# Kernel optimization log

Measured on AMD Instinct MI355X. Metric: run time of the kernel, lower is better.

## Reference

```python
import jax, jax.numpy as jnp
import numpy as np

T_CONST = 0.1

def _hardtanh(w):
    # F.hardtanh(w, min_val=1e-10, max_val=1)
    return jnp.clip(w, 1e-10, 1.0)

def _forward(inp, hn, w_str2str, w_str2snr, w_m12m1, w_m12str, w_thal2m1,
             w_m12thal, w_thal2str, w_str2stn, w_stn2snr, w_snr2thal,
             str2str_fixed, inp_weight, mean_w, mean_b, std_w, std_b, hid_dim):
    H = hid_dim
    H5 = 5 * H
    Z = jnp.zeros((H, H), dtype=inp.dtype)
    n_inhib = int(0.3 * H)

    # Diagonal 'D' matrices realized as column scalings (D is diagonal)
    m12m1_d = jnp.concatenate([jnp.ones((H - n_inhib,)), -jnp.ones((n_inhib,))])

    # Block masks
    str2str_mask = jnp.zeros((H, H))
    m12str_mask = jnp.concatenate([jnp.ones((H, H - n_inhib)), jnp.zeros((H, n_inhib))], axis=1)
    str2stn_mask = jnp.concatenate([jnp.zeros((H, H // 2)), jnp.ones((H, H // 2))], axis=1)
    str2snr_mask = jnp.concatenate([jnp.ones((H, H // 2)), jnp.zeros((H, H // 2))], axis=1)

    # Region masks over the full 5H state
    thal_mask = jnp.concatenate([jnp.zeros((3 * H,)), jnp.ones((H,)), jnp.zeros((H,))])
    m1_mask = jnp.zeros((H5,))  # cat(zeros(4H), zeros(H)) in the source

    # Effective recurrent blocks (str2str_D = stn2snr_D = snr2thal_D = str2snr_D = -I)
    str2str_rec = -(str2str_mask * _hardtanh(w_str2str) + str2str_fixed)
    m12m1_rec = _hardtanh(w_m12m1) * m12m1_d[None, :]
    m12str_rec = m12str_mask * _hardtanh(w_m12str)
    str2snr_rec = -(str2snr_mask * _hardtanh(w_str2snr))
    thal2m1_rec = _hardtanh(w_thal2m1)
    m12thal_rec = _hardtanh(w_m12thal)
    thal2str_rec = _hardtanh(w_thal2str)
    str2stn_rec = str2stn_mask * _hardtanh(w_str2stn)
    stn2snr_rec = -_hardtanh(w_str2stn)  # NOTE: source uses str2stn weight here (faithful to original)
    snr2thal_rec = -_hardtanh(w_snr2thal)

    W_rec = jnp.concatenate([
        jnp.concatenate([str2str_rec, Z, Z, thal2str_rec, m12str_rec], axis=1),
        jnp.concatenate([str2stn_rec, Z, Z, Z, Z], axis=1),
        jnp.concatenate([str2snr_rec, stn2snr_rec, Z, Z, Z], axis=1),
        jnp.concatenate([Z, Z, snr2thal_rec, Z, m12thal_rec], axis=1),
        jnp.concatenate([Z, Z, Z, thal2m1_rec, m12m1_rec], axis=1),
    ], axis=0)  # [5H, 5H]

    # Precompute masked input drive for all timesteps: [T, B, 5H]
    u = jnp.einsum('bti,ih->tbh', inp, _hardtanh(inp_weight)) * thal_mask

    W_rec_T = W_rec.T

    def step(h, u_t):
        # (W_rec @ h.T).T == h @ W_rec.T
        h_new = jax.nn.relu((1.0 - T_CONST) * h + T_CONST * (h @ W_rec_T + u_t))
        return h_new, h_new

    _, hs = jax.lax.scan(step, hn[0], u)  # hs: [T, B, 5H]
    rnn_out = jnp.transpose(hs, (1, 0, 2))  # [B, T, 5H]
    hn_last = rnn_out[:, -1, :][None]  # [1, B, 5H]

    masked = rnn_out * m1_mask
    mean_out = masked @ mean_w + mean_b
    std_out = jnp.clip(masked @ std_w + std_b, -5.0, 10.0)
    return mean_out, std_out, rnn_out, hn_last


def setup_inputs() -> dict:
    H, B, T, I, A = 256, 64, 512, 4, 1
    H5 = 5 * H
    key = jax.random.key(0)
    ks = jax.random.split(key, 20)
    u01 = lambda k, shape, s: jax.random.uniform(k, shape, dtype=jnp.float32) * s
    inputs = {
        'inp': jax.random.uniform(ks[0], (B, T, I), dtype=jnp.float32),
        'hn': jnp.zeros((1, B, H5), dtype=jnp.float32),
        'w_str2str': u01(ks[1], (H, H), 0.01),
        'w_str2snr': u01(ks[2], (H, H), 0.01),
        'w_m12m1': u01(ks[3], (H, H), 0.01),
        'w_m12str': u01(ks[4], (H, H), 0.01),
        'w_thal2m1': u01(ks[5], (H, H), 0.01),
        'w_m12thal': u01(ks[6], (H, H), 0.01),
        'w_thal2str': u01(ks[7], (H, H), 0.01),
        'w_str2stn': u01(ks[8], (H, H), 0.01),
        'w_stn2snr': u01(ks[9], (H, H), 0.01),
        'w_snr2thal': u01(ks[10], (H, H), 0.01),
        'inp_weight': u01(ks[12], (I, H5), 0.1),
        'mean_w': jax.random.normal(ks[13], (H5, A), dtype=jnp.float32) * 0.02,
        'mean_b': jnp.zeros((A,), dtype=jnp.float32),
        'std_w': jax.random.normal(ks[14], (H5, A), dtype=jnp.float32) * 0.02,
        'std_b': jnp.zeros((A,), dtype=jnp.float32),
        'hid_dim': H,
    }
    keep = jax.random.bernoulli(ks[11], 0.15, (H, H)).astype(jnp.float32)
    inputs['str2str_fixed'] = u01(ks[15], (H, H), 0.01) * keep
    return inputs


def reference(inp, hn, w_str2str, w_str2snr, w_m12m1, w_m12str, w_thal2m1,
              w_m12thal, w_thal2str, w_str2stn, w_stn2snr, w_snr2thal,
              str2str_fixed, inp_weight, mean_w, mean_b, std_w, std_b, hid_dim):
    return _forward(inp, hn, w_str2str, w_str2snr, w_m12m1, w_m12str, w_thal2m1,
                    w_m12thal, w_thal2str, w_str2stn, w_stn2snr, w_snr2thal,
                    str2str_fixed, inp_weight, mean_w, mean_b, std_w, std_b, hid_dim)
```

## Files before the change

### kernel.cpp

```cpp
#include <hip/hip_runtime.h>

typedef unsigned short u16;
typedef unsigned long long u64;
typedef __bf16 v8bf __attribute__((ext_vector_type(8)));
typedef float f32x4 __attribute__((ext_vector_type(4)));
typedef u16 u16x4 __attribute__((ext_vector_type(4)));

#define H5 1280
#define TT 512
#define NBLK 80
#define SPL 81920

#define OFF_W0 0
#define OFF_W1 3276800
#define OFF_W2 6553600
#define OFF_HS 9830400
#define OFF_WIN 10813440
#define OFF_CNT 10817536

#define MFMA(a, b, c) __builtin_amdgcn_mfma_f32_16x16x32_bf16(a, b, c, 0, 0, 0)

__device__ __forceinline__ float htanh_(float x) {
  return fminf(fmaxf(x, 1e-10f), 1.0f);
}
__device__ __forceinline__ u16 f2b(float f) {
  unsigned u = __float_as_uint(f);
  return (u16)((u + 0x7fffu + ((u >> 16) & 1u)) >> 16);
}
__device__ __forceinline__ float b2f(u16 b) {
  return __uint_as_float(((unsigned)b) << 16);
}

__device__ __forceinline__ v8bf ldh(const u16* p) {
  union { u64 q[2]; v8bf v; } u;
  u.q[0] = __hip_atomic_load((const u64*)p, __ATOMIC_RELAXED, __HIP_MEMORY_SCOPE_AGENT);
  u.q[1] = __hip_atomic_load((const u64*)(p + 4), __ATOMIC_RELAXED, __HIP_MEMORY_SCOPE_AGENT);
  return u.v;
}
__device__ __forceinline__ void sth(u16* p, u16x4 v) {
  union { u16x4 s; u64 q; } u;
  u.s = v;
  __hip_atomic_store((u64*)p, u.q, __ATOMIC_RELAXED, __HIP_MEMORY_SCOPE_AGENT);
}

__global__ void build_w(const float* __restrict__ w_str2snr, const float* __restrict__ w_m12m1,
                        const float* __restrict__ w_m12str, const float* __restrict__ w_thal2m1,
                        const float* __restrict__ w_m12thal, const float* __restrict__ w_thal2str,
                        const float* __restrict__ w_str2stn, const float* __restrict__ w_snr2thal,
                        const float* __restrict__ fixedw, u16* __restrict__ W0,
                        u16* __restrict__ W1, u16* __restrict__ W2) {
  int idx = blockIdx.x * 256 + threadIdx.x;
  if (idx >= H5 * H5) return;
  int j = idx / H5, k = idx - j * H5;
  int jr = j >> 8, kr = k >> 8, kk = k & 255;
  int o = (j & 255) * 256 + kk;
  float w = 0.0f;
  if (jr == 0) {
    if (kr == 0) w = -fixedw[o];
    else if (kr == 3) w = htanh_(w_thal2str[o]);
    else if (kr == 4) w = (kk < 180) ? htanh_(w_m12str[o]) : 0.0f;
  } else if (jr == 1) {
    if (kr == 0) w = (kk >= 128) ? htanh_(w_str2stn[o]) : 0.0f;
  } else if (jr == 2) {
    if (kr == 0) w = (kk < 128) ? -htanh_(w_str2snr[o]) : 0.0f;
    else if (kr == 1) w = -htanh_(w_str2stn[o]);
  } else if (jr == 3) {
    if (kr == 2) w = -htanh_(w_snr2thal[o]);
    else if (kr == 4) w = htanh_(w_m12thal[o]);
  } else {
    if (kr == 3) w = htanh_(w_thal2m1[o]);
    else if (kr == 4) w = (kk < 180) ? htanh_(w_m12m1[o]) : -htanh_(w_m12m1[o]);
  }
  u16 c0 = f2b(w);  float r1 = w - b2f(c0);
  u16 c1 = f2b(r1); float r2 = r1 - b2f(c1);
  u16 c2 = f2b(r2);
  W0[idx] = c0; W1[idx] = c1; W2[idx] = c2;
}

__global__ void build_misc(const float* __restrict__ hn, const float* __restrict__ inp_weight,
                           const float* __restrict__ mean_b, const float* __restrict__ std_b,
                           float* __restrict__ out, u16* __restrict__ hs, float* __restrict__ Win) {
  int gid = blockIdx.x * 256 + threadIdx.x;
  if (gid < 65536) {
    out[gid] = (gid < 32768) ? mean_b[0] : fminf(10.0f, fmaxf(-5.0f, std_b[0]));
  } else if (gid < 65536 + SPL) {
    int i = gid - 65536;
    float v = hn[i];
    u16 c0 = f2b(v);  float r1 = v - b2f(c0);
    u16 c1 = f2b(r1); float r2 = r1 - b2f(c1);
    u16 c2 = f2b(r2);
    hs[i] = c0; hs[SPL + i] = c1; hs[2 * SPL + i] = c2;
  } else if (gid < 65536 + SPL + 1024) {
    int i = gid - 65536 - SPL;
    Win[i] = htanh_(inp_weight[(i >> 8) * H5 + 768 + (i & 255)]);
  }
}

template <int R> struct RC;
template <> struct RC<0> { static constexpr int kb[3] = {0, 768, 1024}; static constexpr int nch[3] = {8, 8, 8}; };
template <> struct RC<1> { static constexpr int kb[3] = {128, 0, 0};    static constexpr int nch[3] = {4, 0, 0}; };
template <> struct RC<2> { static constexpr int kb[3] = {0, 256, 0};    static constexpr int nch[3] = {4, 8, 0}; };
template <> struct RC<3> { static constexpr int kb[3] = {512, 1024, 0}; static constexpr int nch[3] = {8, 8, 0}; };
template <> struct RC<4> { static constexpr int kb[3] = {768, 1024, 0}; static constexpr int nch[3] = {8, 8, 0}; };
template <int R> constexpr int NCT = RC<R>::nch[0] + RC<R>::nch[1] + RC<R>::nch[2];

template <int R>
__device__ __forceinline__ void load_afr_t(const u16* __restrict__ W0, const u16* __restrict__ W1,
                                           const u16* __restrict__ W2, int j0, int lr, int lk,
                                           v8bf (&afr)[NCT<R>][3]) {
  const long jrow = (long)(j0 + lr) * H5 + lk;
  int idx = 0;
#pragma unroll
  for (int q = 0; q < 3; ++q) {
#pragma unroll
    for (int c = 0; c < RC<R>::nch[q]; ++c) {
      long off = jrow + RC<R>::kb[q] + c * 32;
      afr[idx][0] = *(const v8bf*)(W0 + off);
      afr[idx][1] = *(const v8bf*)(W1 + off);
      afr[idx][2] = *(const v8bf*)(W2 + off);
      ++idx;
    }
  }
}

template <int R>
__device__ __forceinline__ f32x4 mfma_step_t(const u16* __restrict__ hs_r, int b, int lk,
                                             const v8bf (&afr)[NCT<R>][3]) {
  f32x4 a00 = {0.f, 0.f, 0.f, 0.f}, a01 = {0.f, 0.f, 0.f, 0.f};
  f32x4 a10 = {0.f, 0.f, 0.f, 0.f}, a11 = {0.f, 0.f, 0.f, 0.f};
  int idx = 0;
#pragma unroll
  for (int q = 0; q < 3; ++q) {
    if (RC<R>::nch[q] > 0) {
      const u16* hb = hs_r + (long)b * H5 + RC<R>::kb[q] + lk;
#pragma unroll
      for (int c = 0; c < RC<R>::nch[q]; ++c) {
        v8bf h0 = ldh(hb + c * 32);
        v8bf h1 = ldh(hb + SPL + c * 32);
        v8bf h2 = ldh(hb + 2 * SPL + c * 32);
        if (idx & 1) {
          a10 = MFMA(afr[idx][0], h0, a10);
          a11 = MFMA(afr[idx][0], h1, a11);
          a10 = MFMA(afr[idx][1], h0, a10);
          a11 = MFMA(afr[idx][1], h1, a11);
          a10 = MFMA(afr[idx][2], h0, a10);
          a11 = MFMA(afr[idx][0], h2, a11);
        } else {
          a00 = MFMA(afr[idx][0], h0, a00);
          a01 = MFMA(afr[idx][0], h1, a01);
          a00 = MFMA(afr[idx][1], h0, a00);
          a01 = MFMA(afr[idx][1], h1, a01);
          a00 = MFMA(afr[idx][2], h0, a00);
          a01 = MFMA(afr[idx][0], h2, a01);
        }
        ++idx;
      }
    }
  }
  f32x4 acc;
#pragma unroll
  for (int rr = 0; rr < 4; ++rr) acc[rr] = (a00[rr] + a01[rr]) + (a10[rr] + a11[rr]);
  return acc;
}

template <int R>
__device__ void pers_loop(int j0, int b, int lr, int hi, int lk,
                          const float* __restrict__ inp_b, const float* __restrict__ hn,
                          const u16* __restrict__ W0, const u16* __restrict__ W1,
                          const u16* __restrict__ W2, u16* __restrict__ hs,
                          float* __restrict__ rnn_b, float* __restrict__ hn_last,
                          const float* __restrict__ Win, unsigned* __restrict__ counter) {
  v8bf afr[NCT<R>][3];
  load_afr_t<R>(W0, W1, W2, j0, lr, lk, afr);

  float winreg[4][4];
  if constexpr (R == 3) {
#pragma unroll
    for (int i = 0; i < 4; ++i)
#pragma unroll
      for (int rr = 0; rr < 4; ++rr)
        winreg[i][rr] = Win[i * 256 + (j0 - 768) + hi * 4 + rr];
  }

  f32x4 hprev;
  {
    const float* hp = hn + (long)b * H5 + j0 + hi * 4;
#pragma unroll
    for (int rr = 0; rr < 4; ++rr) hprev[rr] = hp[rr];
  }

  const u64 ca = (u64)counter;

  for (int t = 0; t < TT; ++t) {
    const u16* hs_r = hs + (t & 1) * (3 * SPL);
    u16* hs_w = hs + ((t & 1) ^ 1) * (3 * SPL);

    f32x4 acc = mfma_step_t<R>(hs_r, b, lk, afr);

    if constexpr (R == 3) {
      const float* ip = inp_b + t * 4;
      float i0 = ip[0], i1 = ip[1], i2 = ip[2], i3 = ip[3];
#pragma unroll
      for (int rr = 0; rr < 4; ++rr)
        acc[rr] += i0 * winreg[0][rr] + i1 * winreg[1][rr] + i2 * winreg[2][rr] + i3 * winreg[3][rr];
    }

    f32x4 hnew;
#pragma unroll
    for (int rr = 0; rr < 4; ++rr)
      hnew[rr] = fmaxf(0.0f, 0.9f * hprev[rr] + 0.1f * acc[rr]);
    hprev = hnew;

    *(f32x4*)(rnn_b + (long)t * H5 + j0 + hi * 4) = hnew;

    if (t < TT - 1) {
      u16x4 s0, s1, s2;
#pragma unroll
      for (int rr = 0; rr < 4; ++rr) {
        float v = hnew[rr];
        u16 c0 = f2b(v);  float r1 = v - b2f(c0);
        u16 c1 = f2b(r1); float r2 = r1 - b2f(c1);
        s0[rr] = c0; s1[rr] = c1; s2[rr] = f2b(r2);
      }
      u16* hw = hs_w + (long)b * H5 + j0 + hi * 4;
      sth(hw, s0);
      sth(hw + SPL, s1);
      sth(hw + 2 * SPL, s2);

      asm volatile("s_waitcnt vmcnt(0)" ::: "memory");
      __syncthreads();
      if (threadIdx.x == 0) {
        unsigned old;
        asm volatile("global_atomic_add %0, %1, %2, off sc0 sc1\n\t"
                     "s_waitcnt vmcnt(0)"
                     : "=v"(old) : "v"(ca), "v"(1u) : "memory");
        const unsigned target = (unsigned)(t + 1) * NBLK;
        for (;;) {
          unsigned cur;
          asm volatile("global_load_dword %0, %1, off sc0 sc1\n\t"
                       "s_waitcnt vmcnt(0)"
                       : "=v"(cur) : "v"(ca) : "memory");
          if (cur >= target) break;
          __builtin_amdgcn_s_sleep(1);
        }
      }
      __syncthreads();
    } else {
      float* hl = hn_last + (long)b * H5 + j0 + hi * 4;
#pragma unroll
      for (int rr = 0; rr < 4; ++rr) hl[rr] = hnew[rr];
    }
  }
}

__global__ void __launch_bounds__(256, 1)
rnn_pers(const float* __restrict__ inp, const float* __restrict__ hn,
         const u16* __restrict__ W0, const u16* __restrict__ W1, const u16* __restrict__ W2,
         u16* __restrict__ hs, float* __restrict__ rnn, float* __restrict__ hn_last,
         const float* __restrict__ Win, unsigned* __restrict__ counter) {
  const int lane = threadIdx.x & 63;
  const int lr = lane & 15, hi = lane >> 4, lk = hi * 8;
  const int jt = blockIdx.x;
  const int bt = threadIdx.x >> 6;
  const int j0 = jt << 4;
  const int b = (bt << 4) + lr;
  float* rnn_b = rnn + (long)b * TT * H5;
  const float* inp_b = inp + (long)b * TT * 4;
  switch (jt >> 4) {
    case 0: pers_loop<0>(j0, b, lr, hi, lk, inp_b, hn, W0, W1, W2, hs, rnn_b, hn_last, Win, counter); break;
    case 1: pers_loop<1>(j0, b, lr, hi, lk, inp_b, hn, W0, W1, W2, hs, rnn_b, hn_last, Win, counter); break;
    case 2: pers_loop<2>(j0, b, lr, hi, lk, inp_b, hn, W0, W1, W2, hs, rnn_b, hn_last, Win, counter); break;
    case 3: pers_loop<3>(j0, b, lr, hi, lk, inp_b, hn, W0, W1, W2, hs, rnn_b, hn_last, Win, counter); break;
    default: pers_loop<4>(j0, b, lr, hi, lk, inp_b, hn, W0, W1, W2, hs, rnn_b, hn_last, Win, counter); break;
  }
}

template <int R>
__device__ void step_one(int t, int j0, int b, int lr, int hi, int lk,
                         const float* __restrict__ inp_b, const float* __restrict__ hn,
                         const u16* __restrict__ W0, const u16* __restrict__ W1,
                         const u16* __restrict__ W2, u16* __restrict__ hs,
                         float* __restrict__ rnn, float* __restrict__ rnn_b,
                         float* __restrict__ hn_last, const float* __restrict__ Win) {
  v8bf afr[NCT<R>][3];
  load_afr_t<R>(W0, W1, W2, j0, lr, lk, afr);
  float winreg[4][4];
  if constexpr (R == 3) {
#pragma unroll
    for (int i = 0; i < 4; ++i)
#pragma unroll
      for (int rr = 0; rr < 4; ++rr)
        winreg[i][rr] = Win[i * 256 + (j0 - 768) + hi * 4 + rr];
  }
  f32x4 hprev;
  {
    const float* hp = (t == 0) ? (hn + (long)b * H5 + j0 + hi * 4)
                               : (rnn + ((long)b * TT + (t - 1)) * H5 + j0 + hi * 4);
#pragma unroll
    for (int rr = 0; rr < 4; ++rr) hprev[rr] = hp[rr];
  }
  const u16* hs_r = hs + (t & 1) * (3 * SPL);
  u16* hs_w = hs + ((t & 1) ^ 1) * (3 * SPL);

  f32x4 acc = mfma_step_t<R>(hs_r, b, lk, afr);
  if constexpr (R == 3) {
    const float* ip = inp_b + t * 4;
    float i0 = ip[0], i1 = ip[1], i2 = ip[2], i3 = ip[3];
#pragma unroll
    for (int rr = 0; rr < 4; ++rr)
      acc[rr] += i0 * winreg[0][rr] + i1 * winreg[1][rr] + i2 * winreg[2][rr] + i3 * winreg[3][rr];
  }
  f32x4 hnew;
#pragma unroll
  for (int rr = 0; rr < 4; ++rr)
    hnew[rr] = fmaxf(0.0f, 0.9f * hprev[rr] + 0.1f * acc[rr]);

  *(f32x4*)(rnn_b + (long)t * H5 + j0 + hi * 4) = hnew;
  if (t < TT - 1) {
    u16x4 s0, s1, s2;
#pragma unroll
    for (int rr = 0; rr < 4; ++rr) {
      float v = hnew[rr];
      u16 c0 = f2b(v);  float r1 = v - b2f(c0);
      u16 c1 = f2b(r1); float r2 = r1 - b2f(c1);
      s0[rr] = c0; s1[rr] = c1; s2[rr] = f2b(r2);
    }
    u16* hw = hs_w + (long)b * H5 + j0 + hi * 4;
    sth(hw, s0);
    sth(hw + SPL, s1);
    sth(hw + 2 * SPL, s2);
  } else {
    float* hl = hn_last + (long)b * H5 + j0 + hi * 4;
#pragma unroll
    for (int rr = 0; rr < 4; ++rr) hl[rr] = hnew[rr];
  }
}

__global__ void __launch_bounds__(256, 1)
rnn_step(const float* __restrict__ inp, const float* __restrict__ hn,
         const u16* __restrict__ W0, const u16* __restrict__ W1, const u16* __restrict__ W2,
         u16* __restrict__ hs, float* __restrict__ rnn, float* __restrict__ hn_last,
         const float* __restrict__ Win, int t) {
  const int lane = threadIdx.x & 63;
  const int lr = lane & 15, hi = lane >> 4, lk = hi * 8;
  const int jt = blockIdx.x;
  const int bt = threadIdx.x >> 6;
  const int j0 = jt << 4;
  const int b = (bt << 4) + lr;
  float* rnn_b = rnn + (long)b * TT * H5;
  const float* inp_b = inp + (long)b * TT * 4;
  switch (jt >> 4) {
    case 0: step_one<0>(t, j0, b, lr, hi, lk, inp_b, hn, W0, W1, W2, hs, rnn, rnn_b, hn_last, Win); break;
    case 1: step_one<1>(t, j0, b, lr, hi, lk, inp_b, hn, W0, W1, W2, hs, rnn, rnn_b, hn_last, Win); break;
    case 2: step_one<2>(t, j0, b, lr, hi, lk, inp_b, hn, W0, W1, W2, hs, rnn, rnn_b, hn_last, Win); break;
    case 3: step_one<3>(t, j0, b, lr, hi, lk, inp_b, hn, W0, W1, W2, hs, rnn, rnn_b, hn_last, Win); break;
    default: step_one<4>(t, j0, b, lr, hi, lk, inp_b, hn, W0, W1, W2, hs, rnn, rnn_b, hn_last, Win); break;
  }
}

extern "C" void kernel_launch(void* const* d_in, const int* in_sizes, int n_in,
                              void* d_out, int out_size, void* d_ws, size_t ws_size,
                              hipStream_t stream) {
  const float* inp        = (const float*)d_in[0];
  const float* hn         = (const float*)d_in[1];
  const float* w_str2snr  = (const float*)d_in[3];
  const float* w_m12m1    = (const float*)d_in[4];
  const float* w_m12str   = (const float*)d_in[5];
  const float* w_thal2m1  = (const float*)d_in[6];
  const float* w_m12thal  = (const float*)d_in[7];
  const float* w_thal2str = (const float*)d_in[8];
  const float* w_str2stn  = (const float*)d_in[9];
  const float* w_snr2thal = (const float*)d_in[11];
  const float* inp_weight = (const float*)d_in[12];
  const float* mean_b     = (const float*)d_in[14];
  const float* std_b      = (const float*)d_in[16];
  const float* fixedw     = (const float*)d_in[18];

  char* ws = (char*)d_ws;
  u16* W0 = (u16*)(ws + OFF_W0);
  u16* W1 = (u16*)(ws + OFF_W1);
  u16* W2 = (u16*)(ws + OFF_W2);
  u16* hsb = (u16*)(ws + OFF_HS);
  float* Win = (float*)(ws + OFF_WIN);
  unsigned* cnt = (unsigned*)(ws + OFF_CNT);

  float* out = (float*)d_out;
  float* rnn = out + 65536;
  float* hnl = out + 65536 + 41943040;

  hipMemsetAsync(cnt, 0, 128, stream);
  build_w<<<6400, 256, 0, stream>>>(w_str2snr, w_m12m1, w_m12str, w_thal2m1, w_m12thal,
                                    w_thal2str, w_str2stn, w_snr2thal, fixedw, W0, W1, W2);
  build_misc<<<581, 256, 0, stream>>>(hn, inp_weight, mean_b, std_b, out, hsb, Win);

  void* args[] = {(void*)&inp, (void*)&hn, (void*)&W0, (void*)&W1, (void*)&W2, (void*)&hsb,
                  (void*)&rnn, (void*)&hnl, (void*)&Win, (void*)&cnt};
  hipError_t e = hipLaunchCooperativeKernel((const void*)rnn_pers, dim3(NBLK), dim3(256),
                                            args, 0, stream);
  if (e != hipSuccess) {
    for (int t = 0; t < TT; ++t)
      rnn_step<<<NBLK, 256, 0, stream>>>(inp, hn, W0, W1, W2, hsb, rnn, hnl, Win, t);
  }
}
```

Before: 10.02 ms.

## Stream weight fragments from memory each step instead of holding them in registers

Measured after the change: 10.20 ms. No clear change (+1.8%).

```diff
diff --git a/kernel.cpp b/kernel.cpp
--- a/kernel.cpp
+++ b/kernel.cpp
@@ -31,7 +31,7 @@
   return __uint_as_float(((unsigned)b) << 16);
 }
 
-__device__ __forceinline__ v8bf ldh(const u16* p) {
+__device__ __forceinline__ v8bf ald16(const u16* p) {
   union { u64 q[2]; v8bf v; } u;
   u.q[0] = __hip_atomic_load((const u64*)p, __ATOMIC_RELAXED, __HIP_MEMORY_SCOPE_AGENT);
   u.q[1] = __hip_atomic_load((const u64*)(p + 4), __ATOMIC_RELAXED, __HIP_MEMORY_SCOPE_AGENT);
@@ -102,64 +102,39 @@
 template <> struct RC<2> { static constexpr int kb[3] = {0, 256, 0};    static constexpr int nch[3] = {4, 8, 0}; };
 template <> struct RC<3> { static constexpr int kb[3] = {512, 1024, 0}; static constexpr int nch[3] = {8, 8, 0}; };
 template <> struct RC<4> { static constexpr int kb[3] = {768, 1024, 0}; static constexpr int nch[3] = {8, 8, 0}; };
-template <int R> constexpr int NCT = RC<R>::nch[0] + RC<R>::nch[1] + RC<R>::nch[2];
 
 template <int R>
-__device__ __forceinline__ void load_afr_t(const u16* __restrict__ W0, const u16* __restrict__ W1,
-                                           const u16* __restrict__ W2, int j0, int lr, int lk,
-                                           v8bf (&afr)[NCT<R>][3]) {
-  const long jrow = (long)(j0 + lr) * H5 + lk;
-  int idx = 0;
-#pragma unroll
-  for (int q = 0; q < 3; ++q) {
-#pragma unroll
-    for (int c = 0; c < RC<R>::nch[q]; ++c) {
-      long off = jrow + RC<R>::kb[q] + c * 32;
-      afr[idx][0] = *(const v8bf*)(W0 + off);
-      afr[idx][1] = *(const v8bf*)(W1 + off);
-      afr[idx][2] = *(const v8bf*)(W2 + off);
-      ++idx;
-    }
-  }
-}
-
-template <int R>
-__device__ __forceinline__ f32x4 mfma_step_t(const u16* __restrict__ hs_r, int b, int lk,
-                                             const v8bf (&afr)[NCT<R>][3]) {
-  f32x4 a00 = {0.f, 0.f, 0.f, 0.f}, a01 = {0.f, 0.f, 0.f, 0.f};
-  f32x4 a10 = {0.f, 0.f, 0.f, 0.f}, a11 = {0.f, 0.f, 0.f, 0.f};
-  int idx = 0;
+__device__ __forceinline__ f32x4 do_mm(const u16* __restrict__ hs_r, int b, int lk,
+                                       const u16* __restrict__ w0r, const u16* __restrict__ w1r,
+                                       const u16* __restrict__ w2r) {
+  f32x4 A00 = {0.f, 0.f, 0.f, 0.f}, A01 = {0.f, 0.f, 0.f, 0.f}, A02 = {0.f, 0.f, 0.f, 0.f};
+  f32x4 A10 = {0.f, 0.f, 0.f, 0.f}, A11 = {0.f, 0.f, 0.f, 0.f}, A20 = {0.f, 0.f, 0.f, 0.f};
 #pragma unroll
   for (int q = 0; q < 3; ++q) {
     if (RC<R>::nch[q] > 0) {
-      const u16* hb = hs_r + (long)b * H5 + RC<R>::kb[q] + lk;
+      const int kbq = RC<R>::kb[q];
+      const u16* hb = hs_r + (long)b * H5 + kbq + lk;
 #pragma unroll
       for (int c = 0; c < RC<R>::nch[q]; ++c) {
-        v8bf h0 = ldh(hb + c * 32);
-        v8bf h1 = ldh(hb + SPL + c * 32);
-        v8bf h2 = ldh(hb + 2 * SPL + c * 32);
-        if (idx & 1) {
-          a10 = MFMA(afr[idx][0], h0, a10);
-          a11 = MFMA(afr[idx][0], h1, a11);
-          a10 = MFMA(afr[idx][1], h0, a10);
-          a11 = MFMA(afr[idx][1], h1, a11);
-          a10 = MFMA(afr[idx][2], h0, a10);
-          a11 = MFMA(afr[idx][0], h2, a11);
-        } else {
-          a00 = MFMA(afr[idx][0], h0, a00);
-          a01 = MFMA(afr[idx][0], h1, a01);
-          a00 = MFMA(afr[idx][1], h0, a00);
-          a01 = MFMA(afr[idx][1], h1, a01);
-          a00 = MFMA(afr[idx][2], h0, a00);
-          a01 = MFMA(afr[idx][0], h2, a01);
-        }
-        ++idx;
+        v8bf h0 = ald16(hb + c * 32);
+        v8bf h1 = ald16(hb + SPL + c * 32);
+        v8bf h2 = ald16(hb + 2 * SPL + c * 32);
+        v8bf a0 = *(const v8bf*)(w0r + kbq + c * 32);
+        v8bf a1 = *(const v8bf*)(w1r + kbq + c * 32);
+        v8bf a2 = *(const v8bf*)(w2r + kbq + c * 32);
+        A00 = MFMA(a0, h0, A00);
+        A01 = MFMA(a0, h1, A01);
+        A02 = MFMA(a0, h2, A02);
+        A10 = MFMA(a1, h0, A10);
+        A11 = MFMA(a1, h1, A11);
+        A20 = MFMA(a2, h0, A20);
       }
     }
   }
   f32x4 acc;
 #pragma unroll
-  for (int rr = 0; rr < 4; ++rr) acc[rr] = (a00[rr] + a01[rr]) + (a10[rr] + a11[rr]);
+  for (int rr = 0; rr < 4; ++rr)
+    acc[rr] = ((A00[rr] + A10[rr]) + (A01[rr] + A11[rr])) + (A02[rr] + A20[rr]);
   return acc;
 }
 
@@ -170,8 +145,10 @@
                           const u16* __restrict__ W2, u16* __restrict__ hs,
                           float* __restrict__ rnn_b, float* __restrict__ hn_last,
                           const float* __restrict__ Win, unsigned* __restrict__ counter) {
-  v8bf afr[NCT<R>][3];
-  load_afr_t<R>(W0, W1, W2, j0, lr, lk, afr);
+  const long jrow = (long)(j0 + lr) * H5 + lk;
+  const u16* w0r = W0 + jrow;
+  const u16* w1r = W1 + jrow;
+  const u16* w2r = W2 + jrow;
 
   float winreg[4][4];
   if constexpr (R == 3) {
@@ -195,7 +172,7 @@
     const u16* hs_r = hs + (t & 1) * (3 * SPL);
     u16* hs_w = hs + ((t & 1) ^ 1) * (3 * SPL);
 
-    f32x4 acc = mfma_step_t<R>(hs_r, b, lk, afr);
+    f32x4 acc = do_mm<R>(hs_r, b, lk, w0r, w1r, w2r);
 
     if constexpr (R == 3) {
       const float* ip = inp_b + t * 4;
@@ -282,33 +259,32 @@
                          const u16* __restrict__ W2, u16* __restrict__ hs,
                          float* __restrict__ rnn, float* __restrict__ rnn_b,
                          float* __restrict__ hn_last, const float* __restrict__ Win) {
-  v8bf afr[NCT<R>][3];
-  load_afr_t<R>(W0, W1, W2, j0, lr, lk, afr);
-  float winreg[4][4];
+  const long jrow = (long)(j0 + lr) * H5 + lk;
+  const u16* hs_r = hs + (t & 1) * (3 * SPL);
+  u16* hs_w = hs + ((t & 1) ^ 1) * (3 * SPL);
+
+  f32x4 acc = do_mm<R>(hs_r, b, lk, W0 + jrow, W1 + jrow, W2 + jrow);
+
   if constexpr (R == 3) {
+    float winreg[4][4];
 #pragma unroll
     for (int i = 0; i < 4; ++i)
 #pragma unroll
       for (int rr = 0; rr < 4; ++rr)
         winreg[i][rr] = Win[i * 256 + (j0 - 768) + hi * 4 + rr];
-  }
+    const float* ip = inp_b + t * 4;
+    float i0 = ip[0], i1 = ip[1], i2 = ip[2], i3 = ip[3];
+#pragma unroll
+    for (int rr = 0; rr < 4; ++rr)
+      acc[rr] += i0 * winreg[0][rr] + i1 * winreg[1][rr] + i2 * winreg[2][rr] + i3 * winreg[3][rr];
+  }
+
   f32x4 hprev;
   {
     const float* hp = (t == 0) ? (hn + (long)b * H5 + j0 + hi * 4)
                                : (rnn + ((long)b * TT + (t - 1)) * H5 + j0 + hi * 4);
 #pragma unroll
     for (int rr = 0; rr < 4; ++rr) hprev[rr] = hp[rr];
-  }
-  const u16* hs_r = hs + (t & 1) * (3 * SPL);
-  u16* hs_w = hs + ((t & 1) ^ 1) * (3 * SPL);
-
-  f32x4 acc = mfma_step_t<R>(hs_r, b, lk, afr);
-  if constexpr (R == 3) {
-    const float* ip = inp_b + t * 4;
-    float i0 = ip[0], i1 = ip[1], i2 = ip[2], i3 = ip[3];
-#pragma unroll
-    for (int rr = 0; rr < 4; ++rr)
-      acc[rr] += i0 * winreg[0][rr] + i1 * winreg[1][rr] + i2 * winreg[2][rr] + i3 * winreg[3][rr];
   }
   f32x4 hnew;
 #pragma unroll
```
